# Performance work log

Hardware: AMD Instinct MI355X
Metric: run time of the kernel (lower is better)

The kernel has to match this reference:

```python
import jax, jax.numpy as jnp
import numpy as np

D_MODEL = 1024
N_HEADS = 16
HEAD_DIM = D_MODEL // N_HEADS
Q_PROJ = D_MODEL // 2
KV_PROJ = D_MODEL
INIT_SCALE = 0.02
EPS = 1e-5


def _ln(x, g, b):
    mu = jnp.mean(x, axis=-1, keepdims=True)
    var = jnp.mean(jnp.square(x - mu), axis=-1, keepdims=True)
    return (x - mu) * jax.lax.rsqrt(var + EPS) * g + b


def setup_inputs() -> dict:
    key = jax.random.key(0)
    ks = jax.random.split(key, 8)
    B, S = 2, 2048
    x = jax.random.normal(ks[0], (B, S, D_MODEL), dtype=jnp.float32)
    W_dq = INIT_SCALE * jax.random.normal(ks[1], (D_MODEL, Q_PROJ), dtype=jnp.float32)
    W_uq = INIT_SCALE * jax.random.normal(ks[2], (Q_PROJ, D_MODEL), dtype=jnp.float32)
    W_dkv = INIT_SCALE * jax.random.normal(ks[3], (D_MODEL, KV_PROJ), dtype=jnp.float32)
    W_ukv = INIT_SCALE * jax.random.normal(ks[4], (KV_PROJ, 2 * D_MODEL), dtype=jnp.float32)
    wo = INIT_SCALE * jax.random.normal(ks[5], (D_MODEL, D_MODEL), dtype=jnp.float32)
    return {
        "x": x,
        "W_dq": W_dq, "W_uq": W_uq,
        "q_ln_g": jnp.ones((Q_PROJ,), jnp.float32), "q_ln_b": jnp.zeros((Q_PROJ,), jnp.float32),
        "W_dkv": W_dkv, "W_ukv": W_ukv,
        "kv_ln_g": jnp.ones((KV_PROJ,), jnp.float32), "kv_ln_b": jnp.zeros((KV_PROJ,), jnp.float32),
        "preq_g": jnp.ones((D_MODEL,), jnp.float32), "preq_b": jnp.zeros((D_MODEL,), jnp.float32),
        "prekv_g": jnp.ones((D_MODEL,), jnp.float32), "prekv_b": jnp.zeros((D_MODEL,), jnp.float32),
        "wo": wo,
    }


def reference(x, W_dq, W_uq, q_ln_g, q_ln_b, W_dkv, W_ukv, kv_ln_g, kv_ln_b,
              preq_g, preq_b, prekv_g, prekv_b, wo):
    B, S, D = x.shape
    H, dh = N_HEADS, HEAD_DIM
    # Q path: pre-norm -> low-rank down -> LN -> up
    x_q = _ln(x, preq_g, preq_b)
    cq = _ln(x_q @ W_dq, q_ln_g, q_ln_b)            # [B,S,D/2]
    Q = (cq @ W_uq).reshape(B, S, H, dh)             # [B,S,H,dh]
    Q = Q / jnp.sqrt(jnp.asarray(dh, x.dtype))
    # KV path: pre-norm -> compress -> LN -> up, split into K,V
    x_kv = _ln(x, prekv_g, prekv_b)
    ckv = _ln(x_kv @ W_dkv, kv_ln_g, kv_ln_b)        # [B,S,D]
    KV = ckv @ W_ukv                                 # [B,S,2D]
    K, V = jnp.split(KV, 2, axis=-1)
    K = K.reshape(B, S, H, dh)
    V = V.reshape(B, S, H, dh)
    # causal attention (scores materialized as in original)
    scores = jnp.einsum('bqhd,bkhd->bhqk', Q, K)     # [B,H,S,S]
    causal = jnp.tril(jnp.ones((S, S), dtype=bool))  # True where allowed
    scores = jnp.where(causal[None, None], scores, jnp.asarray(-jnp.inf, scores.dtype))
    attn = jax.nn.softmax(scores, axis=-1)
    out = jnp.einsum('bhqk,bkhd->bqhd', attn, V).reshape(B, S, D)
    return out @ wo.T
```

## Files before the change

kernel.cpp:

```cpp
#include <hip/hip_runtime.h>
#include <hip/hip_bf16.h>

#define SEQ   2048
#define BATCH 2
#define NROWS 4096
#define DM    1024
#define NHEAD 16
#define DH    64
#define QP    512
#define KVP   1024

typedef unsigned short us;
typedef ushort4 us4;
using bf16x8 = __attribute__((ext_vector_type(8))) __bf16;
using f32x4  = __attribute__((ext_vector_type(4))) float;

__device__ __forceinline__ us f2bf(float f) {
  union { __hip_bfloat16 h; us u; } cv;
  cv.h = __float2bfloat16(f);
  return cv.u;
}
__device__ __forceinline__ float bf2f(us u) {
  union { unsigned int u32; float f; } cv;
  cv.u32 = ((unsigned int)u) << 16;
  return cv.f;
}
__device__ __forceinline__ float loadp(const void* p, long i, int isbf) {
  return isbf ? bf2f(((const us*)p)[i]) : ((const float*)p)[i];
}
__device__ __forceinline__ void async16(const void* g, void* l) {
  __builtin_amdgcn_global_load_lds((__attribute__((address_space(1))) void*)g,
                                   (__attribute__((address_space(3))) void*)l,
                                   16, 0, 0);
}
__device__ __forceinline__ unsigned cvtpk(float lo, float hi) {
  unsigned r;
  asm("v_cvt_pk_bf16_f32 %0, %1, %2" : "=v"(r) : "v"(lo), "v"(hi));
  return r;
}

__global__ void detect_dtype(const us* __restrict__ xu, int* __restrict__ flag) {
  __shared__ int red[256];
  const int tid = threadIdx.x;
  int cnt = 0;
  for (int i = tid; i < 4096; i += 256) {
    const int e = (xu[i] >> 7) & 0xff;
    if (e == 0 || (e >= 100 && e <= 134)) cnt++;
  }
  red[tid] = cnt;
  __syncthreads();
  for (int s = 128; s; s >>= 1) {
    if (tid < s) red[tid] += red[tid + s];
    __syncthreads();
  }
  if (tid == 0) *flag = (red[0] >= 3900) ? 1 : 0;
}

struct TD { const void* in; us* out; int R, C, nt, trans; };

__global__ __launch_bounds__(256) void stage0(
    TD t0, TD t1, TD t2, TD t3, TD t4,
    const void* __restrict__ xin,
    const void* __restrict__ g1, const void* __restrict__ b1,
    const void* __restrict__ g2, const void* __restrict__ b2,
    us* __restrict__ out1, us* __restrict__ out2,
    const int* __restrict__ flag)
{
  __shared__ us tile[32][33];
  __shared__ float red[8];
  __shared__ float musd[2];
  const int tid = threadIdx.x;
  const int isbf = *flag;
  int lin = blockIdx.x;

  if (lin < 5120) {
    TD t = t0;
    if (lin >= t.nt) { lin -= t.nt; t = t1;
      if (lin >= t.nt) { lin -= t.nt; t = t2;
        if (lin >= t.nt) { lin -= t.nt; t = t3;
          if (lin >= t.nt) { lin -= t.nt; t = t4; } } } }
    const int ntx = t.C >> 5;
    const int by = lin / ntx, bx = lin - by * ntx;
    const int tx = tid & 31, ty = tid >> 5;
    const long r0 = (long)by * 32, c0 = (long)bx * 32;
    if (t.trans) {
#pragma unroll
      for (int i = 0; i < 32; i += 8)
        tile[ty + i][tx] = isbf ? ((const us*)t.in)[(r0 + ty + i) * t.C + c0 + tx]
                                : f2bf(((const float*)t.in)[(r0 + ty + i) * t.C + c0 + tx]);
      __syncthreads();
#pragma unroll
      for (int i = 0; i < 32; i += 8)
        t.out[(c0 + ty + i) * t.R + r0 + tx] = tile[tx][ty + i];
    } else {
#pragma unroll
      for (int i = 0; i < 32; i += 8)
        t.out[(r0 + ty + i) * t.C + c0 + tx] =
            isbf ? ((const us*)t.in)[(r0 + ty + i) * t.C + c0 + tx]
                 : f2bf(((const float*)t.in)[(r0 + ty + i) * t.C + c0 + tx]);
    }
    return;
  }
  const long row = lin - 5120;
  float v[4];
  float s = 0.f, s2 = 0.f;
#pragma unroll
  for (int i = 0; i < 4; i++) {
    const long c = tid + i * 256;
    const float t = loadp(xin, row * 1024 + c, isbf);
    v[i] = t; s += t; s2 += t * t;
  }
#pragma unroll
  for (int off = 32; off > 0; off >>= 1) {
    s  += __shfl_down(s,  off);
    s2 += __shfl_down(s2, off);
  }
  const int wave = tid >> 6, lane = tid & 63;
  if (lane == 0) { red[wave] = s; red[4 + wave] = s2; }
  __syncthreads();
  if (tid == 0) {
    const float ts = red[0] + red[1] + red[2] + red[3];
    const float t2 = red[4] + red[5] + red[6] + red[7];
    const float mu = ts * (1.f / 1024.f);
    const float var = t2 * (1.f / 1024.f) - mu * mu;
    musd[0] = mu; musd[1] = rsqrtf(var + 1e-5f);
  }
  __syncthreads();
  const float mu = musd[0], rs = musd[1];
#pragma unroll
  for (int i = 0; i < 4; i++) {
    const long c = tid + i * 256;
    const float nrm = (v[i] - mu) * rs;
    out1[row * 1024 + c] = f2bf(nrm * loadp(g1, c, isbf) + loadp(b1, c, isbf));
    out2[row * 1024 + c] = f2bf(nrm * loadp(g2, c, isbf) + loadp(b2, c, isbf));
  }
}

template<int C>
__device__ __forceinline__ void ln_body(const us* __restrict__ in,
                                        const void* __restrict__ g, const void* __restrict__ b,
                                        us* __restrict__ out, long row, int tid, int isbf) {
  constexpr int NP = C / 256;
  float v[NP];
  float s = 0.f, s2 = 0.f;
#pragma unroll
  for (int i = 0; i < NP; i++) {
    const float t = bf2f(in[row * C + tid + i * 256]);
    v[i] = t; s += t; s2 += t * t;
  }
#pragma unroll
  for (int off = 32; off > 0; off >>= 1) {
    s  += __shfl_down(s,  off);
    s2 += __shfl_down(s2, off);
  }
  __shared__ float red[8];
  __shared__ float musd[2];
  const int wave = tid >> 6, lane = tid & 63;
  if (lane == 0) { red[wave] = s; red[4 + wave] = s2; }
  __syncthreads();
  if (tid == 0) {
    const float ts = red[0] + red[1] + red[2] + red[3];
    const float t2 = red[4] + red[5] + red[6] + red[7];
    const float mu = ts * (1.f / C);
    const float var = t2 * (1.f / C) - mu * mu;
    musd[0] = mu; musd[1] = rsqrtf(var + 1e-5f);
  }
  __syncthreads();
  const float mu = musd[0], rs = musd[1];
#pragma unroll
  for (int i = 0; i < NP; i++) {
    const long c = tid + i * 256;
    out[row * C + c] = f2bf((v[i] - mu) * rs * loadp(g, c, isbf) + loadp(b, c, isbf));
  }
}

__global__ __launch_bounds__(256) void ln_rows_pair(
    const us* __restrict__ inq, const void* __restrict__ qg, const void* __restrict__ qb,
    us* __restrict__ outq,
    const us* __restrict__ inkv, const void* __restrict__ kvg, const void* __restrict__ kvb,
    us* __restrict__ outkv,
    const int* __restrict__ flag)
{
  const int isbf = *flag;
  if (blockIdx.x < NROWS)
    ln_body<512>(inq, qg, qb, outq, blockIdx.x, threadIdx.x, isbf);
  else
    ln_body<1024>(inkv, kvg, kvb, outkv, blockIdx.x - NROWS, threadIdx.x, isbf);
}

struct GD { const us* A; const us* Bt; void* C; int N, K, nxs; float scale; int omode; };

__global__ __launch_bounds__(256) void gemm_mt(GD g0, GD g1, int nb0,
                                               const int* __restrict__ flag) {
  __shared__ us As[2][128 * 32];
  __shared__ us Bs[2][128 * 32];
  GD g;
  int lin = blockIdx.x;
  {
    const int cpx = gridDim.x >> 3;
    lin = (lin & 7) * cpx + (lin >> 3);
  }
  if (lin < nb0) g = g0; else { g = g1; lin -= nb0; }
  const int by = lin >> g.nxs;
  const int bx = lin - (by << g.nxs);
  const int N = g.N, K = g.K;

  const int tid  = threadIdx.x;
  const int lane = tid & 63;
  const int wave = tid >> 6;
  const int n16  = lane & 15;
  const int quad = lane >> 4;
  const long m0 = (long)by * 128;
  const long n0 = (long)bx * 128;
  const int wm = (wave >> 1) * 64;
  const int wn = (wave & 1) * 64;

  const f32x4 zero = {0.f, 0.f, 0.f, 0.f};
  f32x4 acc[4][4];
#pragma unroll
  for (int i = 0; i < 4; i++)
#pragma unroll
    for (int j = 0; j < 4; j++) acc[i][j] = zero;

  const int srow = tid >> 2;
  const int scol = (tid & 3) * 8;
  const us* Ag0 = g.A  + (m0 + srow) * K + scol;
  const us* Ag1 = g.A  + (m0 + 64 + srow) * K + scol;
  const us* Bg0 = g.Bt + (n0 + srow) * K + scol;
  const us* Bg1 = g.Bt + (n0 + 64 + srow) * K + scol;
  const int lds_off = srow * 32 + scol;

  for (int k0 = 0; k0 < K; k0 += 64) {
#pragma unroll
    for (int s = 0; s < 2; s++) {
      const int ks = k0 + s * 32;
      async16(Ag0 + ks, As[s] + lds_off);
      async16(Ag1 + ks, As[s] + 2048 + lds_off);
      async16(Bg0 + ks, Bs[s] + lds_off);
      async16(Bg1 + ks, Bs[s] + 2048 + lds_off);
    }
    __syncthreads();
#pragma unroll
    for (int s = 0; s < 2; s++) {
      bf16x8 af[4], bfv[4];
#pragma unroll
      for (int i = 0; i < 4; i++)
        af[i] = *(const bf16x8*)(As[s] + (wm + i * 16 + n16) * 32 + quad * 8);
#pragma unroll
      for (int j = 0; j < 4; j++)
        bfv[j] = *(const bf16x8*)(Bs[s] + (wn + j * 16 + n16) * 32 + quad * 8);
#pragma unroll
      for (int i = 0; i < 4; i++)
#pragma unroll
        for (int j = 0; j < 4; j++)
          acc[i][j] = __builtin_amdgcn_mfma_f32_16x16x32_bf16(af[i], bfv[j], acc[i][j], 0, 0, 0);
    }
    __syncthreads();
  }

  const bool obf = (g.omode == 1) || (g.omode == 2 && *flag != 0);
  float* Cf = (float*)g.C;
  us* Cb = (us*)g.C;
#pragma unroll
  for (int i = 0; i < 4; i++) {
    const long row = m0 + wm + i * 16 + quad * 4;
#pragma unroll
    for (int j = 0; j < 4; j++) {
      const long col = n0 + wn + j * 16 + n16;
#pragma unroll
      for (int r = 0; r < 4; r++) {
        const float v = acc[i][j][r] * g.scale;
        if (obf) Cb[(row + r) * N + col] = f2bf(v);
        else     Cf[(row + r) * N + col] = v;
      }
    }
  }
}

#define SWZ(row, col) ((row) * 64 + ((col) ^ (((row) & 7) << 3)))

__global__ __launch_bounds__(256, 4) void flash_attn(
    const us* __restrict__ Q, const us* __restrict__ KV,
    us* __restrict__ O)
{
  __shared__ us Ks[64 * 64];
  __shared__ us Vt[64 * 64];

  const int l   = (int)blockIdx.x;
  const int g8  = l & 7;
  const int j   = l >> 3;
  const int a   = j & 15;
  const int cq  = j >> 4;
  const int combo = g8 * 4 + cq;
  const int h   = combo & 15;
  const int bb  = combo >> 4;

  const int tid = threadIdx.x;
  const int lane = tid & 63;
  const int wave = tid >> 6;
  const int n16 = lane & 15;
  const int quad = lane >> 4;
  const long rowQ0 = (long)bb * SEQ;

  const f32x4 zero = {0.f, 0.f, 0.f, 0.f};

  const int kk_key = tid >> 3;
  const int kk_d8  = (tid & 7) * 8;
  const int vd  = tid & 63;
  const int vw  = tid >> 6;
  const int vkb = vw * 8;

  const us* kgb = KV + (rowQ0 + kk_key) * 2048 + h * DH + kk_d8;
  const us* vgb = KV + (rowQ0 + vw * 4) * 2048 + KVP + h * DH + vd;

  uint4 kpre0, kpre1;
  us vraw[16];
  auto loadKV = [&](int kt) {
    const us* kg = kgb + (long)kt * (64 * 2048);
    kpre0 = *(const uint4*)kg;
    kpre1 = *(const uint4*)(kg + 32 * 2048);
    const us* vg = vgb + (long)kt * (64 * 2048);
#pragma unroll
    for (int r = 0; r < 4; r++) {
      vraw[r]      = vg[r * 2048];
      vraw[4 + r]  = vg[(16 + r) * 2048];
      vraw[8 + r]  = vg[(32 + r) * 2048];
      vraw[12 + r] = vg[(48 + r) * 2048];
    }
  };

  for (int ph = 0; ph < 2; ph++) {
    const int qt = ph ? (31 - a) : a;
    const int nt = qt + 1;
    const int qbase = qt * 64;

    bf16x8 aq[2];
    {
      const long gq = (rowQ0 + qbase + wave * 16 + n16) * DM + h * DH;
      aq[0] = *(const bf16x8*)(Q + gq + quad * 8);
      aq[1] = *(const bf16x8*)(Q + gq + 32 + quad * 8);
    }

    f32x4 oacc[4];
#pragma unroll
    for (int d = 0; d < 4; d++) oacc[d] = zero;
    float rsum = 0.f;

    loadKV(0);

    for (int kt = 0; kt < nt; kt++) {
      __syncthreads();
      *(uint4*)(Ks + SWZ(kk_key, kk_d8))      = kpre0;
      *(uint4*)(Ks + SWZ(kk_key + 32, kk_d8)) = kpre1;
      {
        uint4 p0, p1;
        p0.x = (unsigned)vraw[0]  | ((unsigned)vraw[1]  << 16);
        p0.y = (unsigned)vraw[2]  | ((unsigned)vraw[3]  << 16);
        p0.z = (unsigned)vraw[4]  | ((unsigned)vraw[5]  << 16);
        p0.w = (unsigned)vraw[6]  | ((unsigned)vraw[7]  << 16);
        p1.x = (unsigned)vraw[8]  | ((unsigned)vraw[9]  << 16);
        p1.y = (unsigned)vraw[10] | ((unsigned)vraw[11] << 16);
        p1.z = (unsigned)vraw[12] | ((unsigned)vraw[13] << 16);
        p1.w = (unsigned)vraw[14] | ((unsigned)vraw[15] << 16);
        *(uint4*)(Vt + SWZ(vd, vkb))      = p0;
        *(uint4*)(Vt + SWZ(vd, vkb + 32)) = p1;
      }
      __syncthreads();
      if (kt + 1 < nt) loadKV(kt + 1);

      f32x4 sv[4];
#pragma unroll
      for (int j2 = 0; j2 < 4; j2++) {
        const bf16x8 ak0 = *(const bf16x8*)(Ks + SWZ(j2 * 16 + n16, quad * 8));
        const bf16x8 ak1 = *(const bf16x8*)(Ks + SWZ(j2 * 16 + n16, 32 + quad * 8));
        f32x4 s = zero;
        s = __builtin_amdgcn_mfma_f32_16x16x32_bf16(ak0, aq[0], s, 0, 0, 0);
        s = __builtin_amdgcn_mfma_f32_16x16x32_bf16(ak1, aq[1], s, 0, 0, 0);
        sv[j2] = s;
      }

      if (kt == qt) {
        const int qrl = wave * 16 + n16;
#pragma unroll
        for (int j2 = 0; j2 < 4; j2++) {
          const int kl = j2 * 16 + quad * 4;
#pragma unroll
          for (int r = 0; r < 4; r++)
            sv[j2][r] = (kl + r <= qrl) ? sv[j2][r] : -1e30f;
        }
      }

      unsigned pep[4][2];
#pragma unroll
      for (int j2 = 0; j2 < 4; j2++) {
        const float p0 = __builtin_amdgcn_exp2f(sv[j2][0]);
        const float p1 = __builtin_amdgcn_exp2f(sv[j2][1]);
        const float p2 = __builtin_amdgcn_exp2f(sv[j2][2]);
        const float p3 = __builtin_amdgcn_exp2f(sv[j2][3]);
        rsum += (p0 + p1) + (p2 + p3);
        pep[j2][0] = cvtpk(p0, p1);
        pep[j2][1] = cvtpk(p2, p3);
      }

      __builtin_amdgcn_s_setprio(1);
#pragma unroll
      for (int kc = 0; kc < 2; kc++) {
        union { bf16x8 v; unsigned u[4]; } apu;
        apu.u[0] = pep[2 * kc][0];
        apu.u[1] = pep[2 * kc][1];
        apu.u[2] = pep[2 * kc + 1][0];
        apu.u[3] = pep[2 * kc + 1][1];
#pragma unroll
        for (int d = 0; d < 4; d++) {
          const bf16x8 bv = *(const bf16x8*)(Vt + SWZ(d * 16 + n16, kc * 32 + quad * 8));
          oacc[d] = __builtin_amdgcn_mfma_f32_16x16x32_bf16(apu.v, bv, oacc[d], 0, 0, 0);
        }
      }
      __builtin_amdgcn_s_setprio(0);
    }

    rsum += __shfl_xor(rsum, 16);
    rsum += __shfl_xor(rsum, 32);
    const float inv = 1.f / rsum;

    const long rw0 = rowQ0 + qbase + wave * 16;
#pragma unroll
    for (int r = 0; r < 4; r++) {
      const float invr = __shfl(inv, quad * 4 + r);
      us* dst = O + (rw0 + quad * 4 + r) * DM + h * DH + n16;
#pragma unroll
      for (int d = 0; d < 4; d++)
        dst[d * 16] = f2bf(oacc[d][r] * invr);
    }
    __syncthreads();
  }
}

extern "C" void kernel_launch(void* const* d_in, const int* in_sizes, int n_in,
                              void* d_out, int out_size, void* d_ws, size_t ws_size,
                              hipStream_t stream) {
  const void* x      = d_in[0];
  const void* Wdq    = d_in[1];
  const void* Wuq    = d_in[2];
  const void* qg     = d_in[3];
  const void* qb     = d_in[4];
  const void* Wdkv   = d_in[5];
  const void* Wukv   = d_in[6];
  const void* kvg    = d_in[7];
  const void* kvb    = d_in[8];
  const void* preqg  = d_in[9];
  const void* preqb  = d_in[10];
  const void* prekvg = d_in[11];
  const void* prekvb = d_in[12];
  const void* wo     = d_in[13];

  char* ws = (char*)d_ws;
  const long MB = 1 << 20;
  int* flag   = (int*)ws;
  us* wdq_t   = (us*)(ws + 1 * MB);
  us* wuq_t   = (us*)(ws + 2 * MB);
  us* wdkv_t  = (us*)(ws + 3 * MB);
  us* wukv_t  = (us*)(ws + 5 * MB);
  us* wo_c    = (us*)(ws + 9 * MB);
  us* xq      = (us*)(ws + 11 * MB);
  us* xkv     = (us*)(ws + 19 * MB);
  us* obuf    = (us*)(ws + 27 * MB);
  us* tq_bf   = obuf;
  us* cq      = (us*)(ws + 35 * MB);
  us* qbuf    = (us*)(ws + 39 * MB);
  us* tkv_bf  = qbuf;
  us* ckv     = (us*)(ws + 47 * MB);
  us* kv      = (us*)(ws + 55 * MB);

  {
    static int hflag;
    const long xb = (long)in_sizes[0];
    int known = -1;
    if (xb == (long)BATCH * SEQ * DM * 4) known = 0;
    else if (xb == (long)BATCH * SEQ * DM * 2) known = 1;
    if (known >= 0) {
      hflag = known;
      hipMemcpyAsync(flag, &hflag, sizeof(int), hipMemcpyHostToDevice, stream);
    } else {
      detect_dtype<<<1, 256, 0, stream>>>((const us*)x, flag);
    }
  }

  {
    TD t0 = { Wdq,  wdq_t,  1024,  512,  512, 1 };
    TD t1 = { Wuq,  wuq_t,   512, 1024,  512, 1 };
    TD t2 = { Wdkv, wdkv_t, 1024, 1024, 1024, 1 };
    TD t3 = { Wukv, wukv_t, 1024, 2048, 2048, 1 };
    TD t4 = { wo,   wo_c,   1024, 1024, 1024, 0 };
    stage0<<<9216, 256, 0, stream>>>(t0, t1, t2, t3, t4,
                                     x, preqg, preqb, prekvg, prekvb, xq, xkv, flag);
  }

  {
    GD g0 = { xq,  wdq_t,  tq_bf,   512, 1024, 2, 1.f, 1 };
    GD g1 = { xkv, wdkv_t, tkv_bf, 1024, 1024, 3, 1.f, 1 };
    gemm_mt<<<384, 256, 0, stream>>>(g0, g1, 128, flag);
  }

  ln_rows_pair<<<2 * NROWS, 256, 0, stream>>>(tq_bf, qg, qb, cq, tkv_bf, kvg, kvb, ckv, flag);

  {
    GD g0 = { cq,  wuq_t,  qbuf, 1024,  512, 3, 0.125f * 1.44269504f, 1 };
    GD g1 = { ckv, wukv_t, kv,   2048, 1024, 4, 1.f, 1 };
    gemm_mt<<<768, 256, 0, stream>>>(g0, g1, 256, flag);
  }

  flash_attn<<<512, 256, 0, stream>>>(qbuf, kv, obuf);

  {
    GD g0 = { obuf, wo_c, d_out, 1024, 1024, 3, 1.f, 2 };
    gemm_mt<<<256, 256, 0, stream>>>(g0, g0, 256, flag);
  }
}
```

Measured before the change: 246.7 us.

## Split flash attention q-tiles across two 128-thread blocks

Each 64-row query tile is now split between two blocks of two waves, each handling 32 query rows. The grid doubles to 1024 blocks of 128 threads, and each thread loads twice as much K/V into LDS per tile. The aim is more blocks for better CU occupancy and load balance. In exchange, K/V tiles are fetched and staged into LDS twice as often overall, and register pressure per thread rises.

```diff
diff --git a/kernel.cpp b/kernel.cpp
--- a/kernel.cpp
+++ b/kernel.cpp
@@ -279,53 +279,80 @@
 
 #define SWZ(row, col) ((row) * 64 + ((col) ^ (((row) & 7) << 3)))
 
-__global__ __launch_bounds__(256, 4) void flash_attn(
+__global__ __launch_bounds__(128, 2) void flash_attn(
     const us* __restrict__ Q, const us* __restrict__ KV,
     us* __restrict__ O)
 {
   __shared__ us Ks[64 * 64];
   __shared__ us Vt[64 * 64];
 
-  const int l   = (int)blockIdx.x;
-  const int g8  = l & 7;
-  const int j   = l >> 3;
-  const int a   = j & 15;
-  const int cq  = j >> 4;
+  const int l    = (int)blockIdx.x;
+  const int g8   = l & 7;
+  const int j    = l >> 3;
+  const int a    = j & 15;
+  const int half = (j >> 4) & 1;
+  const int cq   = j >> 5;
   const int combo = g8 * 4 + cq;
-  const int h   = combo & 15;
-  const int bb  = combo >> 4;
-
-  const int tid = threadIdx.x;
+  const int h    = combo & 15;
+  const int bb   = combo >> 4;
+
+  const int tid  = threadIdx.x;
   const int lane = tid & 63;
   const int wave = tid >> 6;
-  const int n16 = lane & 15;
+  const int n16  = lane & 15;
   const int quad = lane >> 4;
   const long rowQ0 = (long)bb * SEQ;
 
   const f32x4 zero = {0.f, 0.f, 0.f, 0.f};
 
-  const int kk_key = tid >> 3;
-  const int kk_d8  = (tid & 7) * 8;
+  const int kk_key = tid >> 1;
+  const int kk_c   = (tid & 1) * 32;
   const int vd  = tid & 63;
-  const int vw  = tid >> 6;
-  const int vkb = vw * 8;
-
-  const us* kgb = KV + (rowQ0 + kk_key) * 2048 + h * DH + kk_d8;
-  const us* vgb = KV + (rowQ0 + vw * 4) * 2048 + KVP + h * DH + vd;
-
-  uint4 kpre0, kpre1;
-  us vraw[16];
+  const int vw2 = tid >> 6;
+
+  const us* kgb  = KV + (rowQ0 + kk_key) * 2048 + h * DH + kk_c;
+  const us* vgb0 = KV + (rowQ0 + vw2 * 4) * 2048 + KVP + h * DH + vd;
+  const us* vgb1 = KV + (rowQ0 + (vw2 + 2) * 4) * 2048 + KVP + h * DH + vd;
+
+  uint4 kpre[4];
+  us vraw[32];
   auto loadKV = [&](int kt) {
     const us* kg = kgb + (long)kt * (64 * 2048);
-    kpre0 = *(const uint4*)kg;
-    kpre1 = *(const uint4*)(kg + 32 * 2048);
-    const us* vg = vgb + (long)kt * (64 * 2048);
+#pragma unroll
+    for (int i = 0; i < 4; i++) kpre[i] = *(const uint4*)(kg + i * 8);
+    const us* vg0 = vgb0 + (long)kt * (64 * 2048);
+    const us* vg1 = vgb1 + (long)kt * (64 * 2048);
 #pragma unroll
     for (int r = 0; r < 4; r++) {
-      vraw[r]      = vg[r * 2048];
-      vraw[4 + r]  = vg[(16 + r) * 2048];
-      vraw[8 + r]  = vg[(32 + r) * 2048];
-      vraw[12 + r] = vg[(48 + r) * 2048];
+      vraw[r]       = vg0[r * 2048];
+      vraw[4 + r]   = vg0[(16 + r) * 2048];
+      vraw[8 + r]   = vg0[(32 + r) * 2048];
+      vraw[12 + r]  = vg0[(48 + r) * 2048];
+      vraw[16 + r]  = vg1[r * 2048];
+      vraw[20 + r]  = vg1[(16 + r) * 2048];
+      vraw[24 + r]  = vg1[(32 + r) * 2048];
+      vraw[28 + r]  = vg1[(48 + r) * 2048];
+    }
+  };
+  auto writeLDS = [&]() {
+#pragma unroll
+    for (int i = 0; i < 4; i++)
+      *(uint4*)(Ks + SWZ(kk_key, kk_c + i * 8)) = kpre[i];
+#pragma unroll
+    for (int wblk = 0; wblk < 2; wblk++) {
+      const int base = wblk * 16;
+      const int vkb = (vw2 + wblk * 2) * 8;
+      uint4 p0, p1;
+      p0.x = (unsigned)vraw[base + 0]  | ((unsigned)vraw[base + 1]  << 16);
+      p0.y = (unsigned)vraw[base + 2]  | ((unsigned)vraw[base + 3]  << 16);
+      p0.z = (unsigned)vraw[base + 4]  | ((unsigned)vraw[base + 5]  << 16);
+      p0.w = (unsigned)vraw[base + 6]  | ((unsigned)vraw[base + 7]  << 16);
+      p1.x = (unsigned)vraw[base + 8]  | ((unsigned)vraw[base + 9]  << 16);
+      p1.y = (unsigned)vraw[base + 10] | ((unsigned)vraw[base + 11] << 16);
+      p1.z = (unsigned)vraw[base + 12] | ((unsigned)vraw[base + 13] << 16);
+      p1.w = (unsigned)vraw[base + 14] | ((unsigned)vraw[base + 15] << 16);
+      *(uint4*)(Vt + SWZ(vd, vkb))      = p0;
+      *(uint4*)(Vt + SWZ(vd, vkb + 32)) = p1;
     }
   };
 
@@ -333,10 +360,11 @@
     const int qt = ph ? (31 - a) : a;
     const int nt = qt + 1;
     const int qbase = qt * 64;
+    const int qloc0 = half * 32 + wave * 16;
 
     bf16x8 aq[2];
     {
-      const long gq = (rowQ0 + qbase + wave * 16 + n16) * DM + h * DH;
+      const long gq = (rowQ0 + qbase + qloc0 + n16) * DM + h * DH;
       aq[0] = *(const bf16x8*)(Q + gq + quad * 8);
       aq[1] = *(const bf16x8*)(Q + gq + 32 + quad * 8);
     }
@@ -350,21 +378,7 @@
 
     for (int kt = 0; kt < nt; kt++) {
       __syncthreads();
-      *(uint4*)(Ks + SWZ(kk_key, kk_d8))      = kpre0;
-      *(uint4*)(Ks + SWZ(kk_key + 32, kk_d8)) = kpre1;
-      {
-        uint4 p0, p1;
-        p0.x = (unsigned)vraw[0]  | ((unsigned)vraw[1]  << 16);
-        p0.y = (unsigned)vraw[2]  | ((unsigned)vraw[3]  << 16);
-        p0.z = (unsigned)vraw[4]  | ((unsigned)vraw[5]  << 16);
-        p0.w = (unsigned)vraw[6]  | ((unsigned)vraw[7]  << 16);
-        p1.x = (unsigned)vraw[8]  | ((unsigned)vraw[9]  << 16);
-        p1.y = (unsigned)vraw[10] | ((unsigned)vraw[11] << 16);
-        p1.z = (unsigned)vraw[12] | ((unsigned)vraw[13] << 16);
-        p1.w = (unsigned)vraw[14] | ((unsigned)vraw[15] << 16);
-        *(uint4*)(Vt + SWZ(vd, vkb))      = p0;
-        *(uint4*)(Vt + SWZ(vd, vkb + 32)) = p1;
-      }
+      writeLDS();
       __syncthreads();
       if (kt + 1 < nt) loadKV(kt + 1);
 
@@ -380,7 +394,7 @@
       }
 
       if (kt == qt) {
-        const int qrl = wave * 16 + n16;
+        const int qrl = qloc0 + n16;
 #pragma unroll
         for (int j2 = 0; j2 < 4; j2++) {
           const int kl = j2 * 16 + quad * 4;
@@ -423,7 +437,7 @@
     rsum += __shfl_xor(rsum, 32);
     const float inv = 1.f / rsum;
 
-    const long rw0 = rowQ0 + qbase + wave * 16;
+    const long rw0 = rowQ0 + qbase + qloc0;
 #pragma unroll
     for (int r = 0; r < 4; r++) {
       const float invr = __shfl(inv, quad * 4 + r);
@@ -510,7 +524,7 @@
     gemm_mt<<<768, 256, 0, stream>>>(g0, g1, 256, flag);
   }
 
-  flash_attn<<<512, 256, 0, stream>>>(qbuf, kv, obuf);
+  flash_attn<<<1024, 128, 0, stream>>>(qbuf, kv, obuf);
 
   {
     GD g0 = { obuf, wo_c, d_out, 1024, 1024, 3, 1.f, 2 };
```

Result: slower. 409.9 us (+66.1%).
